# Kernel optimization log

Hardware: AMD Instinct MI355X
Metric: run time of the kernel (lower is better)

Reference implementation:

```python
import jax, jax.numpy as jnp
import numpy as np
from jax import lax

NR, NC, DI, DO = 2048, 10, 8, 16  # routes, digit caps, in-dim, out-dim

# (t1, a1, b1, a2, b2, t3, a3, b3, a4, b4) piecewise-affine squash constants
PRIM_CONSTS = (-13.46416092, 0.000242759, 0.024488359, 0.002769205, 0.06089699,
               13.23405266, -0.002828244, 0.061313814, -0.000219038, 0.023874787)
DIGIT_CONSTS = (-0.075410217, -0.074520095, 0.349297946, -0.534473989, 0.27196494,
                0.062207676, 0.637642944, 0.295330779, 0.169344703, 0.353784456)


def _piecewise(s, t1, a1, b1, a2, b2, t3, a3, b3, a4, b4):
    # Faithful to the torch loop: new_sorted aliases sorted, so each segment
    # count (i1,i2,i3) is computed on the PARTIALLY-MODIFIED array, and each
    # slice end is idx-1 (off-by-one in the source), last slice ends at n-1.
    n = s.shape[0]
    ar = jnp.arange(n)
    i1 = jnp.sum(s < t1)
    s = jnp.where(ar < i1 - 1, a1 * s + b1, s)
    i2 = jnp.sum(s < 0.0)
    s = jnp.where((ar >= i1) & (ar < i2 - 1), a2 * s + b2, s)
    i3 = jnp.sum(s < t3)
    s = jnp.where((ar >= i2) & (ar < i3 - 1), a3 * s + b3, s)
    s = jnp.where((ar >= i3) & (ar < n - 1), a4 * s + b4, s)
    return s


def _squash_map(x, consts):
    # sort -> piecewise-affine remap -> unsort (one row)
    idx = jnp.argsort(x)
    s = _piecewise(x[idx], *consts)
    return s[jnp.argsort(idx)]


def _conv(x, w, b, stride):
    y = lax.conv_general_dilated(x, w, (stride, stride), 'VALID',
                                 dimension_numbers=('NCHW', 'OIHW', 'NCHW'))
    return y + b[None, :, None, None]


def capsnet_forward(data, conv1_w, conv1_b, prim_w, prim_b, W_dc,
                    dec_w1, dec_b1, dec_w2, dec_b2, dec_w3, dec_b3):
    B = data.shape[0]
    x = jax.nn.relu(_conv(data, conv1_w, conv1_b, 1))          # (B,256,24,24)
    u = _conv(x, prim_w, prim_b, 2).reshape(B, NR, DI)          # (B,2048,8) : 8 caps x 32ch x 8x8
    mag = jax.vmap(lambda r: _squash_map(r, PRIM_CONSTS))(u[:, :, 0])  # (B,2048)
    u_sq = mag[:, :, None] * u                                  # PrimaryCaps.my_squash2
    u_hat = jnp.einsum('rcoi,bri->brco', W_dc, u_sq)            # (B,2048,10,16)

    b_ij = jnp.zeros((NR, NC), dtype=u_hat.dtype)               # routing logits
    for it in range(3):
        c_ij = jax.nn.softmax(b_ij, axis=0)                     # softmax over routes (dim=1 in torch)
        s_j = jnp.einsum('rc,brco->bco', c_ij, u_hat)           # (B,10,16)
        f = jax.vmap(lambda r: _squash_map(r, DIGIT_CONSTS))(s_j[:, :, 0])  # (B,10)
        # torch writes the remapped value back into s_j in place (view aliasing),
        # so component 0 of v_j is f*f while other components are f*s_j
        s_mod = s_j.at[:, :, 0].set(f)
        v_j = f[:, :, None] * s_mod                             # (B,10,16)
        if it < 2:
            a_ij = jnp.einsum('brco,bco->brc', u_hat, v_j)      # agreement
            b_ij = b_ij + a_ij.mean(axis=0)

    # Decoder (reconstruction head)
    classes = jnp.sqrt(jnp.sum(v_j ** 2, axis=2))               # (B,10)
    classes = jax.nn.softmax(classes, axis=0)                   # softmax over batch, as in source
    idx = jnp.argmax(classes, axis=1)                           # (B,)
    masked = jnp.eye(NC, dtype=v_j.dtype)[idx]                  # (B,10) one-hot
    t = (v_j * masked[:, :, None]).reshape(B, -1)               # (B,160)
    h = jax.nn.relu(t @ dec_w1.T + dec_b1)
    h = jax.nn.relu(h @ dec_w2.T + dec_b2)
    recon = jax.nn.sigmoid(h @ dec_w3.T + dec_b3)               # (B,1024) = 32*32*1
    # single-array output: [flattened digit caps | flattened reconstruction]
    return jnp.concatenate([v_j.reshape(B, -1), recon], axis=1)  # (B,1184)


def setup_inputs() -> dict:
    key = jax.random.key(0)
    ks = jax.random.split(key, 12)
    f32 = jnp.float32
    return {
        'data': jax.random.normal(ks[0], (100, 1, 32, 32), f32),
        'conv1_w': jax.random.normal(ks[1], (256, 1, 9, 9), f32) * (1.0 / 9.0),
        'conv1_b': jnp.zeros((256,), f32),
        'prim_w': jax.random.normal(ks[2], (256, 256, 9, 9), f32) * (1.0 / 144.0),
        'prim_b': jnp.zeros((256,), f32),
        'W_dc': jax.random.normal(ks[3], (2048, 10, 16, 8), f32) * 0.05,
        'dec_w1': jax.random.normal(ks[4], (512, 160), f32) * 0.079,
        'dec_b1': jnp.zeros((512,), f32),
        'dec_w2': jax.random.normal(ks[5], (1024, 512), f32) * 0.0442,
        'dec_b2': jnp.zeros((1024,), f32),
        'dec_w3': jax.random.normal(ks[6], (1024, 1024), f32) * 0.03125,
        'dec_b3': jnp.zeros((1024,), f32),
        'train_or_test': 0,
        'epch': 0,
    }


def reference(data, conv1_w, conv1_b, prim_w, prim_b, W_dc,
              dec_w1, dec_b1, dec_w2, dec_b2, dec_w3, dec_b3,
              train_or_test, epch):
    return capsnet_forward(data, conv1_w, conv1_b, prim_w, prim_b, W_dc,
                           dec_w1, dec_b1, dec_w2, dec_b2, dec_w3, dec_b3)
```

## Files before the change

kernel.cpp:

```cpp
#include <hip/hip_runtime.h>
#include <cstdint>
#include <cstddef>


#define BATCH 100

static const size_t OFF_WT   = 0;
static const size_t OFF_X1   = 5308416;
static const size_t OFF_PU   = 20054016;
static const size_t OFF_UHAT = 0;
static const size_t OFF_U    = 33161216;
static const size_t OFF_BIJ  = 32768000;
static const size_t OFF_CIJ  = 32788480;
static const size_t OFF_SP   = 32808960;
static const size_t OFF_VJ   = 33064960;
static const size_t OFF_IDX  = 33080960;
static const size_t OFF_H1   = 33081088;
static const size_t OFF_H2   = 33132288;

#define PT1f -13.46416092f
#define PA1f 0.000242759f
#define PB1f 0.024488359f
#define PA2f 0.002769205f
#define PB2f 0.06089699f
#define PT3f 13.23405266f
#define PA3f -0.002828244f
#define PB3f 0.061313814f
#define PA4f -0.000219038f
#define PB4f 0.023874787f

#define DT1f -0.075410217f
#define DA1f -0.074520095f
#define DB1f 0.349297946f
#define DA2f -0.534473989f
#define DB2f 0.27196494f
#define DT3f 0.062207676f
#define DA3f 0.637642944f
#define DB3f 0.295330779f
#define DA4f 0.169344703f
#define DB4f 0.353784456f

#define XROW(r) ((r) * 12 + ((r) >> 1) * 4)
#define XPH 332
#define XTB 664

__global__ __launch_bounds__(256)
void k_transpose_w(const float* __restrict__ w, float* __restrict__ wt) {
  __shared__ float tile[64 * 82];
  int ci = blockIdx.x, co0 = blockIdx.y * 64, t = threadIdx.x;
  for (int f = t; f < 64 * 81; f += 256) {
    int col = f / 81, tap = f - col * 81;
    tile[col * 82 + tap] = w[(size_t)(co0 + col) * 20736 + (size_t)ci * 81 + tap];
  }
  __syncthreads();
  for (int g = t; g < 64 * 81; g += 256) {
    int tap = g / 64, col = g - tap * 64;
    wt[((size_t)ci * 81 + tap) * 256 + co0 + col] = tile[col * 82 + tap];
  }
}

__global__ __launch_bounds__(256)
void k_conv1(const float* __restrict__ data, const float* __restrict__ cw,
             const float* __restrict__ cb, float* __restrict__ x1) {
  __shared__ float img[1024];
  __shared__ float wl[81 * 32];
  int b = blockIdx.x, cg = blockIdx.y, t = threadIdx.x;
  for (int f = t; f < 1024; f += 256) img[f] = data[(size_t)b * 1024 + f];
  for (int f = t; f < 2592; f += 256) {
    int tap = f >> 5, c = f & 31;
    wl[f] = cw[(size_t)(cg * 32 + c) * 81 + tap];
  }
  __syncthreads();
  for (int task = t; task < 1152; task += 256) {
    int q = task % 144, cq = task / 144;
    int p0 = q * 4, oh = p0 / 24, ow0 = p0 % 24;
    float a[4][4];
#pragma unroll
    for (int i = 0; i < 4; ++i)
#pragma unroll
      for (int j = 0; j < 4; ++j) a[i][j] = 0.f;
    for (int kh = 0; kh < 9; ++kh) {
      const float* ir = &img[(oh + kh) * 32 + ow0];
      const float* wr = &wl[kh * 9 * 32 + cq * 4];
#pragma unroll
      for (int kw = 0; kw < 9; ++kw) {
        float4 wv = *(const float4*)(wr + kw * 32);
#pragma unroll
        for (int j = 0; j < 4; ++j) {
          float xv = ir[kw + j];
          a[0][j] = fmaf(wv.x, xv, a[0][j]);
          a[1][j] = fmaf(wv.y, xv, a[1][j]);
          a[2][j] = fmaf(wv.z, xv, a[2][j]);
          a[3][j] = fmaf(wv.w, xv, a[3][j]);
        }
      }
    }
#pragma unroll
    for (int cc = 0; cc < 4; ++cc) {
      int c = cg * 32 + cq * 4 + cc;
      float bias = cb[c];
      float4 o4 = make_float4(fmaxf(a[cc][0] + bias, 0.f), fmaxf(a[cc][1] + bias, 0.f),
                              fmaxf(a[cc][2] + bias, 0.f), fmaxf(a[cc][3] + bias, 0.f));
      *(float4*)&x1[((size_t)(b * 256 + c) * 24 + oh) * 24 + ow0] = o4;
    }
  }
}

__global__ __launch_bounds__(256) __attribute__((amdgpu_waves_per_eu(4, 4)))
void k_prim(const float* __restrict__ x1, const float* __restrict__ wt,
            float* __restrict__ pu) {
  __shared__ float wsh[81 * 32];
  __shared__ float xsh[4 * XTB];
  int t = threadIdx.x;
  int tb = t >> 6, tl = t & 63;
  int coq = tl >> 3, oh = tl & 7;
  int ci_base = blockIdx.x * 32, cog = blockIdx.y, bq = blockIdx.z;
  int b = bq * 4 + tb;

  int xt0 = t / 72, xm0 = t - xt0 * 72;
  int xr0 = xm0 / 3, xo0 = xm0 - xr0 * 3;
  const float* xg0 = x1 + ((size_t)(bq * 4 + xt0) * 256 + ci_base) * 576 + xr0 * 24 + xo0 * 8;
  float* xl0 = &xsh[xt0 * XTB + XROW(xr0) + xo0 * 4];
  int f1 = t + 256;
  int xt1 = f1 / 72, xm1 = f1 - xt1 * 72;
  int xr1 = xm1 / 3, xo1 = xm1 - xr1 * 3;
  bool hx1 = (t < 32);
  const float* xg1 = x1 + ((size_t)(bq * 4 + xt1) * 256 + ci_base) * 576 + xr1 * 24 + xo1 * 8;
  float* xl1 = &xsh[xt1 * XTB + XROW(xr1) + xo1 * 4];
  const float* wg0 = wt + ((size_t)ci_base * 81 + (t >> 3)) * 256 + cog * 32 + (t & 7) * 4;
  float* wl0 = &wsh[(t >> 3) * 32 + (t & 7) * 4];
  bool hw2 = (t < 136);

  float acc[4][8];
#pragma unroll
  for (int i = 0; i < 4; ++i)
#pragma unroll
    for (int j = 0; j < 8; ++j) acc[i][j] = 0.f;

  float4 pxa0 = *(const float4*)xg0, pxb0 = *(const float4*)(xg0 + 4);
  float4 pxa1, pxb1;
  if (hx1) { pxa1 = *(const float4*)xg1; pxb1 = *(const float4*)(xg1 + 4); }
  float4 pw0 = *(const float4*)wg0;
  float4 pw1 = *(const float4*)(wg0 + 32 * 256);
  float4 pw2;
  if (hw2) pw2 = *(const float4*)(wg0 + 64 * 256);

  const float* xb = &xsh[tb * XTB] + XROW(2 * oh);
  const float* wb = &wsh[coq * 4];

#pragma unroll 1
  for (int ci = ci_base; ci < ci_base + 32; ++ci) {
    __syncthreads();
    *(float4*)xl0        = make_float4(pxa0.x, pxa0.z, pxb0.x, pxb0.z);
    *(float4*)(xl0 + XPH) = make_float4(pxa0.y, pxa0.w, pxb0.y, pxb0.w);
    if (hx1) {
      *(float4*)xl1        = make_float4(pxa1.x, pxa1.z, pxb1.x, pxb1.z);
      *(float4*)(xl1 + XPH) = make_float4(pxa1.y, pxa1.w, pxb1.y, pxb1.w);
    }
    *(float4*)wl0             = pw0;
    *(float4*)(wl0 + 32 * 32) = pw1;
    if (hw2) *(float4*)(wl0 + 64 * 32) = pw2;
    __syncthreads();
    if (ci + 1 < ci_base + 32) {
      xg0 += 576; xg1 += 576; wg0 += 81 * 256;
      pxa0 = *(const float4*)xg0; pxb0 = *(const float4*)(xg0 + 4);
      if (hx1) { pxa1 = *(const float4*)xg1; pxb1 = *(const float4*)(xg1 + 4); }
      pw0 = *(const float4*)wg0;
      pw1 = *(const float4*)(wg0 + 32 * 256);
      if (hw2) pw2 = *(const float4*)(wg0 + 64 * 256);
    }
#pragma unroll
    for (int kh = 0; kh < 9; ++kh) {
      const float* xe = xb + (12 * kh + 4 * (kh >> 1));
      float ew[12], ov[12];
      *(float4*)&ew[0] = *(const float4*)xe;
      *(float4*)&ew[4] = *(const float4*)(xe + 4);
      *(float4*)&ew[8] = *(const float4*)(xe + 8);
      *(float4*)&ov[0] = *(const float4*)(xe + XPH);
      *(float4*)&ov[4] = *(const float4*)(xe + XPH + 4);
      *(float4*)&ov[8] = *(const float4*)(xe + XPH + 8);
      const float* wr = wb + kh * 288;
#pragma unroll
      for (int p = 0; p < 5; ++p) {
        float4 wv = *(const float4*)(wr + p * 64);
#pragma unroll
        for (int j = 0; j < 8; ++j) {
          float xv = ew[p + j];
          acc[0][j] = fmaf(wv.x, xv, acc[0][j]);
          acc[1][j] = fmaf(wv.y, xv, acc[1][j]);
          acc[2][j] = fmaf(wv.z, xv, acc[2][j]);
          acc[3][j] = fmaf(wv.w, xv, acc[3][j]);
        }
      }
#pragma unroll
      for (int p = 0; p < 4; ++p) {
        float4 wv = *(const float4*)(wr + 32 + p * 64);
#pragma unroll
        for (int j = 0; j < 8; ++j) {
          float xv = ov[p + j];
          acc[0][j] = fmaf(wv.x, xv, acc[0][j]);
          acc[1][j] = fmaf(wv.y, xv, acc[1][j]);
          acc[2][j] = fmaf(wv.z, xv, acc[2][j]);
          acc[3][j] = fmaf(wv.w, xv, acc[3][j]);
        }
      }
    }
  }
  float* pp = pu + (((size_t)blockIdx.x * BATCH + b) * 2048 +
                    (cog * 32 + coq * 4) * 8 + oh) * 8;
#pragma unroll
  for (int cc = 0; cc < 4; ++cc) {
    *(float4*)(pp + cc * 64)     = make_float4(acc[cc][0], acc[cc][1], acc[cc][2], acc[cc][3]);
    *(float4*)(pp + cc * 64 + 4) = make_float4(acc[cc][4], acc[cc][5], acc[cc][6], acc[cc][7]);
  }
}

__global__ __launch_bounds__(256)
void k_ured(const float* __restrict__ pu, const float* __restrict__ pb,
            float* __restrict__ u) {
  int g4 = blockIdx.x * 256 + threadIdx.x;
  if (g4 >= 409600) return;
  size_t g = (size_t)g4 * 4;
  const size_t S = 1638400;
  float4 s = *(const float4*)(pu + g);
#pragma unroll
  for (int k = 1; k < 8; ++k) {
    float4 p = *(const float4*)(pu + (size_t)k * S + g);
    s.x += p.x; s.y += p.y; s.z += p.z; s.w += p.w;
  }
  int r = (int)((g >> 3) & 2047);
  float bias = pb[r >> 3];
  float4 o = make_float4(s.x + bias, s.y + bias, s.z + bias, s.w + bias);
  *(float4*)(u + g) = o;
}

__global__ __launch_bounds__(256)
void k_squash(float* __restrict__ u) {
  __shared__ float kv[2048];
  __shared__ int kid[2048];
  __shared__ int red[256];
  int b = blockIdx.x, t = threadIdx.x;
  for (int r = t; r < 2048; r += 256) {
    kv[r] = u[((size_t)b * 2048 + r) * 8];
    kid[r] = r;
  }
  __syncthreads();
  for (int size = 2; size <= 2048; size <<= 1) {
    for (int stride = size >> 1; stride > 0; stride >>= 1) {
#pragma unroll 1
      for (int s = 0; s < 4; ++s) {
        int i = t + s * 256;
        int pos = 2 * i - (i & (stride - 1));
        int q = pos + stride;
        float va = kv[pos], vb = kv[q];
        int ia = kid[pos], ib = kid[q];
        bool gt = (va > vb) || (va == vb && ia > ib);
        bool up = ((pos & size) == 0);
        if (gt == up) { kv[pos] = vb; kv[q] = va; kid[pos] = ib; kid[q] = ia; }
      }
      __syncthreads();
    }
  }
  int loc = 0;
#pragma unroll
  for (int s = 0; s < 8; ++s) loc += (kv[t + s * 256] < PT1f) ? 1 : 0;
  red[t] = loc; __syncthreads();
  for (int off = 128; off; off >>= 1) { if (t < off) red[t] += red[t + off]; __syncthreads(); }
  int i1 = red[0]; __syncthreads();
  float m1v[8];
  loc = 0;
#pragma unroll
  for (int s = 0; s < 8; ++s) {
    int p = t + s * 256;
    float v = kv[p];
    float m = (p < i1 - 1) ? (PA1f * v + PB1f) : v;
    m1v[s] = m;
    loc += (m < 0.f) ? 1 : 0;
  }
  red[t] = loc; __syncthreads();
  for (int off = 128; off; off >>= 1) { if (t < off) red[t] += red[t + off]; __syncthreads(); }
  int i2 = red[0]; __syncthreads();
  float m2v[8];
  loc = 0;
#pragma unroll
  for (int s = 0; s < 8; ++s) {
    int p = t + s * 256;
    float m = (p >= i1 && p < i2 - 1) ? (PA2f * m1v[s] + PB2f) : m1v[s];
    m2v[s] = m;
    loc += (m < PT3f) ? 1 : 0;
  }
  red[t] = loc; __syncthreads();
  for (int off = 128; off; off >>= 1) { if (t < off) red[t] += red[t + off]; __syncthreads(); }
  int i3 = red[0]; __syncthreads();
#pragma unroll
  for (int s = 0; s < 8; ++s) {
    int p = t + s * 256;
    float m = m2v[s];
    m = (p >= i2 && p < i3 - 1) ? (PA3f * m + PB3f) : m;
    m = (p >= i3 && p < 2047) ? (PA4f * m + PB4f) : m;
    int rid = kid[p];
    float* row = u + ((size_t)b * 2048 + rid) * 8;
    float4 lo = *(float4*)row;
    float4 hi = *(float4*)(row + 4);
    lo.x *= m; lo.y *= m; lo.z *= m; lo.w *= m;
    hi.x *= m; hi.y *= m; hi.z *= m; hi.w *= m;
    *(float4*)row = lo;
    *(float4*)(row + 4) = hi;
  }
}

__global__ __launch_bounds__(192)
void k_uhat(const float* __restrict__ Wdc, const float* __restrict__ usq,
            float* __restrict__ uhat) {
  int t = threadIdx.x;
  if (t >= 160) return;
  int r0 = blockIdx.x * 8;
#pragma unroll 1
  for (int half = 0; half < 2; ++half) {
    int rb = r0 + half * 4;
    float4 wa[4], wb4[4];
#pragma unroll
    for (int rl = 0; rl < 4; ++rl) {
      const float* wp = Wdc + ((size_t)(rb + rl) * 160 + t) * 8;
      wa[rl]  = *(const float4*)wp;
      wb4[rl] = *(const float4*)(wp + 4);
    }
#pragma unroll 2
    for (int b = 0; b < BATCH; ++b) {
      const float* ub = usq + ((size_t)b * 2048 + rb) * 8;
      float* op = uhat + ((size_t)b * 2048 + rb) * 160 + t;
#pragma unroll
      for (int rl = 0; rl < 4; ++rl) {
        const float* us = ub + rl * 8;
        float v = us[0] * wa[rl].x + us[1] * wa[rl].y + us[2] * wa[rl].z + us[3] * wa[rl].w +
                  us[4] * wb4[rl].x + us[5] * wb4[rl].y + us[6] * wb4[rl].z + us[7] * wb4[rl].w;
        op[(size_t)rl * 160] = v;
      }
    }
  }
}

__global__ __launch_bounds__(256)
void k_softc(const float* __restrict__ bij, float* __restrict__ cij) {
  __shared__ float red[256];
  int c = blockIdx.x, t = threadIdx.x;
  float m = -3.402823466e38f;
  for (int r = t; r < 2048; r += 256) m = fmaxf(m, bij[r * 10 + c]);
  red[t] = m; __syncthreads();
  for (int off = 128; off; off >>= 1) { if (t < off) red[t] = fmaxf(red[t], red[t + off]); __syncthreads(); }
  m = red[0]; __syncthreads();
  float s = 0.f;
  for (int r = t; r < 2048; r += 256) s += expf(bij[r * 10 + c] - m);
  red[t] = s; __syncthreads();
  for (int off = 128; off; off >>= 1) { if (t < off) red[t] += red[t + off]; __syncthreads(); }
  s = red[0];
  for (int r = t; r < 2048; r += 256) cij[r * 10 + c] = expf(bij[r * 10 + c] - m) / s;
}

__global__ __launch_bounds__(192)
void k_sjpart(const float* __restrict__ cij, const float* __restrict__ uhat,
              float* __restrict__ sp, int it0) {
  __shared__ float cl[1280];
  int b = blockIdx.x, ch = blockIdx.y, t = threadIdx.x;
  if (!it0) {
    for (int f = t; f < 1280; f += 192) cl[f] = cij[(size_t)ch * 1280 + f];
  }
  __syncthreads();
  if (t < 160) {
    int c = t >> 4;
    float acc = 0.f;
    const float* up = uhat + ((size_t)b * 2048 + ch * 128) * 160 + t;
    if (it0) {
      const float cuni = 0.00048828125f;
#pragma unroll 4
      for (int rl = 0; rl < 128; ++rl) acc += cuni * up[(size_t)rl * 160];
    } else {
#pragma unroll 4
      for (int rl = 0; rl < 128; ++rl) acc += cl[rl * 10 + c] * up[(size_t)rl * 160];
    }
    sp[((size_t)b * 16 + ch) * 160 + t] = acc;
  }
}

__global__ __launch_bounds__(192)
void k_sjred(const float* __restrict__ sp, float* __restrict__ vj,
             float* __restrict__ dout, int finalit) {
  __shared__ float sl[160];
  __shared__ float fl[10];
  int b = blockIdx.x, t = threadIdx.x;
  if (t < 160) {
    float a = 0.f;
#pragma unroll
    for (int ch = 0; ch < 16; ++ch) a += sp[((size_t)b * 16 + ch) * 160 + t];
    sl[t] = a;
  }
  __syncthreads();
  if (t == 0) {
    float sv[10]; int rk[10];
    for (int c = 0; c < 10; ++c) sv[c] = sl[c * 16];
    for (int c = 0; c < 10; ++c) {
      int r = 0;
      for (int k = 0; k < 10; ++k)
        r += ((sv[k] < sv[c]) || (sv[k] == sv[c] && k < c)) ? 1 : 0;
      rk[c] = r;
    }
    int i1 = 0;
    for (int c = 0; c < 10; ++c) i1 += (sv[c] < DT1f) ? 1 : 0;
    float m1[10];
    for (int c = 0; c < 10; ++c) m1[c] = (rk[c] < i1 - 1) ? (DA1f * sv[c] + DB1f) : sv[c];
    int i2 = 0;
    for (int c = 0; c < 10; ++c) i2 += (m1[c] < 0.f) ? 1 : 0;
    float m2[10];
    for (int c = 0; c < 10; ++c)
      m2[c] = (rk[c] >= i1 && rk[c] < i2 - 1) ? (DA2f * m1[c] + DB2f) : m1[c];
    int i3 = 0;
    for (int c = 0; c < 10; ++c) i3 += (m2[c] < DT3f) ? 1 : 0;
    for (int c = 0; c < 10; ++c) {
      float m = (rk[c] >= i2 && rk[c] < i3 - 1) ? (DA3f * m2[c] + DB3f) : m2[c];
      m = (rk[c] >= i3 && rk[c] < 9) ? (DA4f * m + DB4f) : m;
      fl[c] = m;
    }
  }
  __syncthreads();
  if (t < 160) {
    int c = t >> 4, o = t & 15;
    float fv = fl[c];
    float v = fv * ((o == 0) ? fv : sl[t]);
    vj[(size_t)b * 160 + t] = v;
    if (finalit) dout[(size_t)b * 1184 + t] = v;
  }
}

__global__ __launch_bounds__(192)
void k_amean(const float* __restrict__ uhat, const float* __restrict__ vj,
             float* __restrict__ bij, int first) {
  __shared__ float vl[16000];
  int t = threadIdx.x, r0 = blockIdx.x * 8;
  for (int f = t; f < 16000; f += 192) vl[f] = vj[f];
  __syncthreads();
  if (t < 160) {
    int c = t >> 4;
    float acc[8];
#pragma unroll
    for (int rl = 0; rl < 8; ++rl) acc[rl] = 0.f;
    const float* up0 = uhat + (size_t)r0 * 160 + t;
#pragma unroll 2
    for (int b = 0; b < BATCH; ++b) {
      float vv = vl[b * 160 + t];
      const float* up = up0 + (size_t)b * 327680;
#pragma unroll
      for (int rl = 0; rl < 8; ++rl)
        acc[rl] = fmaf(up[(size_t)rl * 160], vv, acc[rl]);
    }
#pragma unroll
    for (int rl = 0; rl < 8; ++rl) {
      float a = acc[rl];
      for (int off = 8; off; off >>= 1) a += __shfl_down(a, off, 16);
      if ((t & 15) == 0) {
        int r = r0 + rl;
        float val = a / 100.0f;
        bij[r * 10 + c] = first ? val : (bij[r * 10 + c] + val);
      }
    }
  }
}

__global__ __launch_bounds__(256)
void k_cls(const float* __restrict__ vj, int* __restrict__ idxg) {
  __shared__ float cl[1000];
  __shared__ float cm[10];
  __shared__ float cs[10];
  int t = threadIdx.x;
  for (int f = t; f < 1000; f += 256) {
    int b = f / 10, c = f - b * 10;
    float s = 0.f;
#pragma unroll
    for (int o = 0; o < 16; ++o) {
      float v = vj[(size_t)b * 160 + c * 16 + o];
      s += v * v;
    }
    cl[f] = sqrtf(s);
  }
  __syncthreads();
  if (t < 10) {
    float m = -3.402823466e38f;
    for (int b = 0; b < BATCH; ++b) m = fmaxf(m, cl[b * 10 + t]);
    float s = 0.f;
    for (int b = 0; b < BATCH; ++b) s += expf(cl[b * 10 + t] - m);
    cm[t] = m; cs[t] = s;
  }
  __syncthreads();
  for (int b = t; b < BATCH; b += 256) {
    float best = -1.f; int bi = 0;
    for (int c = 0; c < 10; ++c) {
      float val = expf(cl[b * 10 + c] - cm[c]) / cs[c];
      if (val > best) { best = val; bi = c; }
    }
    idxg[b] = bi;
  }
}

__global__ __launch_bounds__(256)
void k_dec1(const float* __restrict__ w1, const float* __restrict__ b1,
            const float* __restrict__ vj, const int* __restrict__ idxg,
            float* __restrict__ h1) {
  int b = blockIdx.x, t = threadIdx.x;
  int id = idxg[b];
  const float* v = vj + (size_t)b * 160 + id * 16;
  for (int j = t; j < 512; j += 256) {
    float acc = b1[j];
    const float* wr = w1 + (size_t)j * 160 + id * 16;
#pragma unroll
    for (int o = 0; o < 16; ++o) acc += wr[o] * v[o];
    h1[(size_t)b * 512 + j] = fmaxf(acc, 0.f);
  }
}

__global__ __launch_bounds__(256)
void k_dec2(const float* __restrict__ w2, const float* __restrict__ b2,
            const float* __restrict__ h1, float* __restrict__ h2) {
  __shared__ float red[4][64][4];
  int t = threadIdx.x, lane = t & 63, strip = t >> 6;
  int j = blockIdx.x * 64 + lane, bs = blockIdx.y * 4;
  float acc[4] = {0.f, 0.f, 0.f, 0.f};
  const float* wr = w2 + (size_t)j * 512 + strip * 128;
  const float* hb = h1 + (size_t)bs * 512 + strip * 128;
  for (int k4 = 0; k4 < 32; ++k4) {
    float4 wv = *(const float4*)(wr + k4 * 4);
    const float* h0 = hb + k4 * 4;
#pragma unroll
    for (int q = 0; q < 4; ++q) {
      float4 hv = *(const float4*)(h0 + q * 512);
      acc[q] += wv.x * hv.x + wv.y * hv.y + wv.z * hv.z + wv.w * hv.w;
    }
  }
#pragma unroll
  for (int q = 0; q < 4; ++q) red[strip][lane][q] = acc[q];
  __syncthreads();
  if (strip == 0) {
    float bias = b2[j];
#pragma unroll
    for (int q = 0; q < 4; ++q) {
      float tot = red[0][lane][q] + red[1][lane][q] + red[2][lane][q] + red[3][lane][q] + bias;
      h2[(size_t)(bs + q) * 1024 + j] = fmaxf(tot, 0.f);
    }
  }
}

__global__ __launch_bounds__(256)
void k_dec3(const float* __restrict__ w3, const float* __restrict__ b3,
            const float* __restrict__ h2, float* __restrict__ dout) {
  __shared__ float red[4][64][4];
  int t = threadIdx.x, lane = t & 63, strip = t >> 6;
  int j = blockIdx.x * 64 + lane, bs = blockIdx.y * 4;
  float acc[4] = {0.f, 0.f, 0.f, 0.f};
  const float* wr = w3 + (size_t)j * 1024 + strip * 256;
  const float* hb = h2 + (size_t)bs * 1024 + strip * 256;
  for (int k4 = 0; k4 < 64; ++k4) {
    float4 wv = *(const float4*)(wr + k4 * 4);
    const float* h0 = hb + k4 * 4;
#pragma unroll
    for (int q = 0; q < 4; ++q) {
      float4 hv = *(const float4*)(h0 + q * 1024);
      acc[q] += wv.x * hv.x + wv.y * hv.y + wv.z * hv.z + wv.w * hv.w;
    }
  }
#pragma unroll
  for (int q = 0; q < 4; ++q) red[strip][lane][q] = acc[q];
  __syncthreads();
  if (strip == 0) {
    float bias = b3[j];
#pragma unroll
    for (int q = 0; q < 4; ++q) {
      float tot = red[0][lane][q] + red[1][lane][q] + red[2][lane][q] + red[3][lane][q] + bias;
      dout[(size_t)(bs + q) * 1184 + 160 + j] = 1.f / (1.f + expf(-tot));
    }
  }
}

extern "C" void kernel_launch(void* const* d_in, const int* in_sizes, int n_in,
                              void* d_out, int out_size, void* d_ws, size_t ws_size,
                              hipStream_t stream) {
  (void)in_sizes; (void)n_in; (void)out_size; (void)ws_size;
  const float* data = (const float*)d_in[0];
  const float* c1w  = (const float*)d_in[1];
  const float* c1b  = (const float*)d_in[2];
  const float* pw   = (const float*)d_in[3];
  const float* pb   = (const float*)d_in[4];
  const float* Wdc  = (const float*)d_in[5];
  const float* w1   = (const float*)d_in[6];
  const float* b1   = (const float*)d_in[7];
  const float* w2   = (const float*)d_in[8];
  const float* b2   = (const float*)d_in[9];
  const float* w3   = (const float*)d_in[10];
  const float* b3   = (const float*)d_in[11];
  float* out = (float*)d_out;
  float* ws  = (float*)d_ws;

  float* WT   = ws + OFF_WT;
  float* X1   = ws + OFF_X1;
  float* PU   = ws + OFF_PU;
  float* UHAT = ws + OFF_UHAT;
  float* U    = ws + OFF_U;
  float* BIJ  = ws + OFF_BIJ;
  float* CIJ  = ws + OFF_CIJ;
  float* SP   = ws + OFF_SP;
  float* VJ   = ws + OFF_VJ;
  int*   IDX  = (int*)(ws + OFF_IDX);
  float* H1   = ws + OFF_H1;
  float* H2   = ws + OFF_H2;

  k_transpose_w<<<dim3(256, 4), 256, 0, stream>>>(pw, WT);
  k_conv1<<<dim3(BATCH, 8), 256, 0, stream>>>(data, c1w, c1b, X1);
  k_prim<<<dim3(8, 8, 25), 256, 0, stream>>>(X1, WT, PU);
  k_ured<<<1600, 256, 0, stream>>>(PU, pb, U);
  k_squash<<<BATCH, 256, 0, stream>>>(U);
  k_uhat<<<256, 192, 0, stream>>>(Wdc, U, UHAT);

  for (int it = 0; it < 3; ++it) {
    if (it > 0) k_softc<<<10, 256, 0, stream>>>(BIJ, CIJ);
    k_sjpart<<<dim3(BATCH, 16), 192, 0, stream>>>(CIJ, UHAT, SP, it == 0 ? 1 : 0);
    k_sjred<<<BATCH, 192, 0, stream>>>(SP, VJ, out, it == 2 ? 1 : 0);
    if (it < 2) k_amean<<<256, 192, 0, stream>>>(UHAT, VJ, BIJ, it == 0 ? 1 : 0);
  }

  k_cls<<<1, 256, 0, stream>>>(VJ, IDX);
  k_dec1<<<BATCH, 256, 0, stream>>>(w1, b1, VJ, IDX, H1);
  k_dec2<<<dim3(16, 25), 256, 0, stream>>>(w2, b2, H1, H2);
  k_dec3<<<dim3(16, 25), 256, 0, stream>>>(w3, b3, H2, out);
}
```

Before: 1.416 ms.

## Double-buffer shared memory tiles in primary-caps conv to drop one barrier per step

Converts the k_prim input/weight staging from a single LDS buffer with two barriers per input channel into a ping-pong double buffer with one barrier per channel. The next channel's prefetched registers are written into the alternate buffer after compute, so stores no longer wait on a barrier before compute. It also removes the fixed waves_per_eu(4,4) occupancy hint. In exchange it doubles LDS usage (about 31 KB per block), which may limit occupancy.

```diff
diff --git a/kernel.cpp b/kernel.cpp
--- a/kernel.cpp
+++ b/kernel.cpp
@@ -43,6 +43,8 @@
 #define XROW(r) ((r) * 12 + ((r) >> 1) * 4)
 #define XPH 332
 #define XTB 664
+#define XBUF (4 * XTB)
+#define WBUF (81 * 32)
 
 __global__ __launch_bounds__(256)
 void k_transpose_w(const float* __restrict__ w, float* __restrict__ wt) {
@@ -106,11 +108,11 @@
   }
 }
 
-__global__ __launch_bounds__(256) __attribute__((amdgpu_waves_per_eu(4, 4)))
+__global__ __launch_bounds__(256)
 void k_prim(const float* __restrict__ x1, const float* __restrict__ wt,
             float* __restrict__ pu) {
-  __shared__ float wsh[81 * 32];
-  __shared__ float xsh[4 * XTB];
+  __shared__ float wsh[2 * WBUF];
+  __shared__ float xsh[2 * XBUF];
   int t = threadIdx.x;
   int tb = t >> 6, tl = t & 63;
   int coq = tl >> 3, oh = tl & 7;
@@ -120,15 +122,15 @@
   int xt0 = t / 72, xm0 = t - xt0 * 72;
   int xr0 = xm0 / 3, xo0 = xm0 - xr0 * 3;
   const float* xg0 = x1 + ((size_t)(bq * 4 + xt0) * 256 + ci_base) * 576 + xr0 * 24 + xo0 * 8;
-  float* xl0 = &xsh[xt0 * XTB + XROW(xr0) + xo0 * 4];
+  int xoff0 = xt0 * XTB + XROW(xr0) + xo0 * 4;
   int f1 = t + 256;
   int xt1 = f1 / 72, xm1 = f1 - xt1 * 72;
   int xr1 = xm1 / 3, xo1 = xm1 - xr1 * 3;
   bool hx1 = (t < 32);
   const float* xg1 = x1 + ((size_t)(bq * 4 + xt1) * 256 + ci_base) * 576 + xr1 * 24 + xo1 * 8;
-  float* xl1 = &xsh[xt1 * XTB + XROW(xr1) + xo1 * 4];
+  int xoff1 = xt1 * XTB + XROW(xr1) + xo1 * 4;
   const float* wg0 = wt + ((size_t)ci_base * 81 + (t >> 3)) * 256 + cog * 32 + (t & 7) * 4;
-  float* wl0 = &wsh[(t >> 3) * 32 + (t & 7) * 4];
+  int woff = (t >> 3) * 32 + (t & 7) * 4;
   bool hw2 = (t < 136);
 
   float acc[4][8];
@@ -137,31 +139,29 @@
 #pragma unroll
     for (int j = 0; j < 8; ++j) acc[i][j] = 0.f;
 
-  float4 pxa0 = *(const float4*)xg0, pxb0 = *(const float4*)(xg0 + 4);
-  float4 pxa1, pxb1;
-  if (hx1) { pxa1 = *(const float4*)xg1; pxb1 = *(const float4*)(xg1 + 4); }
-  float4 pw0 = *(const float4*)wg0;
-  float4 pw1 = *(const float4*)(wg0 + 32 * 256);
-  float4 pw2;
-  if (hw2) pw2 = *(const float4*)(wg0 + 64 * 256);
-
-  const float* xb = &xsh[tb * XTB] + XROW(2 * oh);
-  const float* wb = &wsh[coq * 4];
+  {
+    float4 a0 = *(const float4*)xg0, b0 = *(const float4*)(xg0 + 4);
+    float* d0 = &xsh[xoff0];
+    *(float4*)d0 = make_float4(a0.x, a0.z, b0.x, b0.z);
+    *(float4*)(d0 + XPH) = make_float4(a0.y, a0.w, b0.y, b0.w);
+    if (hx1) {
+      float4 a1 = *(const float4*)xg1, b1 = *(const float4*)(xg1 + 4);
+      float* d1 = &xsh[xoff1];
+      *(float4*)d1 = make_float4(a1.x, a1.z, b1.x, b1.z);
+      *(float4*)(d1 + XPH) = make_float4(a1.y, a1.w, b1.y, b1.w);
+    }
+    float* wd = &wsh[woff];
+    *(float4*)wd = *(const float4*)wg0;
+    *(float4*)(wd + 32 * 32) = *(const float4*)(wg0 + 32 * 256);
+    if (hw2) *(float4*)(wd + 64 * 32) = *(const float4*)(wg0 + 64 * 256);
+  }
+  __syncthreads();
 
 #pragma unroll 1
-  for (int ci = ci_base; ci < ci_base + 32; ++ci) {
-    __syncthreads();
-    *(float4*)xl0        = make_float4(pxa0.x, pxa0.z, pxb0.x, pxb0.z);
-    *(float4*)(xl0 + XPH) = make_float4(pxa0.y, pxa0.w, pxb0.y, pxb0.w);
-    if (hx1) {
-      *(float4*)xl1        = make_float4(pxa1.x, pxa1.z, pxb1.x, pxb1.z);
-      *(float4*)(xl1 + XPH) = make_float4(pxa1.y, pxa1.w, pxb1.y, pxb1.w);
-    }
-    *(float4*)wl0             = pw0;
-    *(float4*)(wl0 + 32 * 32) = pw1;
-    if (hw2) *(float4*)(wl0 + 64 * 32) = pw2;
-    __syncthreads();
-    if (ci + 1 < ci_base + 32) {
+  for (int k = 0; k < 32; ++k) {
+    int cur = k & 1;
+    float4 pxa0, pxb0, pxa1, pxb1, pw0, pw1, pw2;
+    if (k < 31) {
       xg0 += 576; xg1 += 576; wg0 += 81 * 256;
       pxa0 = *(const float4*)xg0; pxb0 = *(const float4*)(xg0 + 4);
       if (hx1) { pxa1 = *(const float4*)xg1; pxb1 = *(const float4*)(xg1 + 4); }
@@ -169,6 +169,8 @@
       pw1 = *(const float4*)(wg0 + 32 * 256);
       if (hw2) pw2 = *(const float4*)(wg0 + 64 * 256);
     }
+    const float* xb = &xsh[cur * XBUF + tb * XTB] + XROW(2 * oh);
+    const float* wb = &wsh[cur * WBUF + coq * 4];
 #pragma unroll
     for (int kh = 0; kh < 9; ++kh) {
       const float* xe = xb + (12 * kh + 4 * (kh >> 1));
@@ -204,6 +206,22 @@
           acc[3][j] = fmaf(wv.w, xv, acc[3][j]);
         }
       }
+    }
+    if (k < 31) {
+      int nb = (cur ^ 1);
+      float* xd0 = &xsh[nb * XBUF + xoff0];
+      *(float4*)xd0 = make_float4(pxa0.x, pxa0.z, pxb0.x, pxb0.z);
+      *(float4*)(xd0 + XPH) = make_float4(pxa0.y, pxa0.w, pxb0.y, pxb0.w);
+      if (hx1) {
+        float* xd1 = &xsh[nb * XBUF + xoff1];
+        *(float4*)xd1 = make_float4(pxa1.x, pxa1.z, pxb1.x, pxb1.z);
+        *(float4*)(xd1 + XPH) = make_float4(pxa1.y, pxa1.w, pxb1.y, pxb1.w);
+      }
+      float* wd = &wsh[nb * WBUF + woff];
+      *(float4*)wd = pw0;
+      *(float4*)(wd + 32 * 32) = pw1;
+      if (hw2) *(float4*)(wd + 64 * 32) = pw2;
+      __syncthreads();
     }
   }
   float* pp = pu + (((size_t)blockIdx.x * BATCH + b) * 2048 +
```

New measurement: 3.487 ms. +146.2%, slower.
